# Kernel optimization log

Measured on AMD Instinct MI355X. Metric: run time of the kernel, lower is better.

Reference implementation:

```python
import jax, jax.numpy as jnp
import numpy as np

# Model dims (from init_kwargs + mamba_ssm defaults)
D_MODEL = 1024
N_LAYER = 2
D_STATE = 16
D_CONV = 4
D_INNER = 2 * D_MODEL          # expand=2
DT_RANK = D_MODEL // 16        # 64
VOCAB = 32000
BATCH, SEQLEN = 2, 1024


def setup_inputs() -> dict:
    key = jax.random.key(0)
    ks = jax.random.split(key, 10)
    s = 0.02
    x = jax.random.randint(ks[0], (BATCH, SEQLEN), 0, VOCAB)
    embedding = jax.random.normal(ks[1], (VOCAB, D_MODEL), dtype=jnp.float32) * s
    norm_w = jnp.ones((N_LAYER, D_MODEL), dtype=jnp.float32)
    in_proj_w = jax.random.normal(ks[2], (N_LAYER, 2 * D_INNER, D_MODEL), dtype=jnp.float32) * s
    conv_w = jax.random.normal(ks[3], (N_LAYER, D_INNER, D_CONV), dtype=jnp.float32) * (1.0 / np.sqrt(D_CONV))
    conv_b = jnp.zeros((N_LAYER, D_INNER), dtype=jnp.float32)
    x_proj_w = jax.random.normal(ks[4], (N_LAYER, DT_RANK + 2 * D_STATE, D_INNER), dtype=jnp.float32) * s
    dt_proj_w = jax.random.normal(ks[5], (N_LAYER, D_INNER, DT_RANK), dtype=jnp.float32) * (DT_RANK ** -0.5)
    # inverse-softplus of dt_init ~ 0.01 (mamba default dt range)
    dt_bias = jnp.full((N_LAYER, D_INNER), float(np.log(np.expm1(0.01))), dtype=jnp.float32)
    A_log = jnp.log(jnp.broadcast_to(jnp.arange(1, D_STATE + 1, dtype=jnp.float32), (N_LAYER, D_INNER, D_STATE)))
    D = jnp.ones((N_LAYER, D_INNER), dtype=jnp.float32)
    out_proj_w = jax.random.normal(ks[6], (N_LAYER, D_MODEL, D_INNER), dtype=jnp.float32) * s
    final_norm_w = jnp.ones((D_MODEL,), dtype=jnp.float32)
    return {"x": x, "embedding": embedding, "norm_w": norm_w, "in_proj_w": in_proj_w,
            "conv_w": conv_w, "conv_b": conv_b, "x_proj_w": x_proj_w, "dt_proj_w": dt_proj_w,
            "dt_bias": dt_bias, "A_log": A_log, "D": D, "out_proj_w": out_proj_w,
            "final_norm_w": final_norm_w}


def _rmsnorm(h, w, eps=1e-5):
    return h * jax.lax.rsqrt(jnp.mean(h * h, axis=-1, keepdims=True) + eps) * w


def _scan_combine(c1, c2):
    a1, b1 = c1
    a2, b2 = c2
    return a2 * a1, a2 * b1 + b2


def _mamba_block(h, norm_w, in_proj_w, conv_w, conv_b, x_proj_w, dt_proj_w, dt_bias, A_log, D, out_proj_w):
    u = _rmsnorm(h, norm_w)
    xz = jnp.einsum('bld,ed->ble', u, in_proj_w)           # [B,L,2*D_INNER]
    xi, z = jnp.split(xz, 2, axis=-1)
    # depthwise causal conv1d, kernel D_CONV
    k = conv_w.T[:, None, :]                               # [D_CONV, 1, D_INNER]
    xc = jax.lax.conv_general_dilated(xi, k, (1,), [(D_CONV - 1, 0)],
                                      dimension_numbers=('NLC', 'LIO', 'NLC'),
                                      feature_group_count=D_INNER) + conv_b
    xc = jax.nn.silu(xc)
    dbl = jnp.einsum('bld,ed->ble', xc, x_proj_w)          # [B,L,DT_RANK+2*D_STATE]
    dt_low = dbl[..., :DT_RANK]
    Bm = dbl[..., DT_RANK:DT_RANK + D_STATE]
    Cm = dbl[..., DT_RANK + D_STATE:]
    dt = jax.nn.softplus(jnp.einsum('blr,dr->bld', dt_low, dt_proj_w) + dt_bias)
    A = -jnp.exp(A_log)                                    # [D_INNER, D_STATE]
    a = jnp.exp(dt[..., None] * A)                         # [B,L,D_INNER,D_STATE]
    b = dt[..., None] * Bm[:, :, None, :] * xc[..., None]  # [B,L,D_INNER,D_STATE]
    hs = jax.lax.associative_scan(_scan_combine, (a, b), axis=1)[1]
    y = jnp.einsum('bldn,bln->bld', hs, Cm) + xc * D
    y = y * jax.nn.silu(z)
    return h + jnp.einsum('bld,md->blm', y, out_proj_w)


def reference(x, embedding, norm_w, in_proj_w, conv_w, conv_b, x_proj_w, dt_proj_w,
              dt_bias, A_log, D, out_proj_w, final_norm_w):
    h = embedding[x]                                       # [B,L,D_MODEL]
    for i in range(N_LAYER):
        h = _mamba_block(h, norm_w[i], in_proj_w[i], conv_w[i], conv_b[i], x_proj_w[i],
                         dt_proj_w[i], dt_bias[i], A_log[i], D[i], out_proj_w[i])
    h = _rmsnorm(h, final_norm_w)
    logits = jnp.einsum('bld,vd->blv', h, embedding)       # tied lm head
    return logits
```

## Files before the change

kernel.cpp:

```cpp
#include <hip/hip_runtime.h>
#include <hip/hip_bf16.h>
#include <math.h>

#define D_MODEL 1024
#define N_LAYER 2
#define D_STATE 16
#define D_CONV  4
#define D_INNER 2048
#define DT_RANK 64
#define VOCAB   32000
#define BATCH   2
#define SEQLEN  1024
#define TOKENS  (BATCH*SEQLEN)
#define NC      64
#define CL      16
#define XPZ     16

typedef __hip_bfloat16 bf16;
typedef __bf16 bf16x8 __attribute__((ext_vector_type(8)));
typedef float f32x4 __attribute__((ext_vector_type(4)));

__device__ inline void gld_lds16(const bf16* g, bf16* l) {
    __builtin_amdgcn_global_load_lds(
        (const __attribute__((address_space(1))) void*)g,
        (__attribute__((address_space(3))) void*)l, 16, 0, 0);
}

__device__ inline float softplus_fast(float v) {
    return (v > 20.f) ? v : __logf(1.f + __expf(v));
}
__device__ inline float silu_fast(float v) {
    return v / (1.f + __expf(-v));
}
__device__ inline float bfu(unsigned short s) {
    unsigned u = ((unsigned)s) << 16;
    float f;
    __builtin_memcpy(&f, &u, 4);
    return f;
}

__global__ __launch_bounds__(256) void embed_rms(const int* __restrict__ x,
                                                 const float* __restrict__ emb,
                                                 const float* __restrict__ w,
                                                 float* __restrict__ h,
                                                 bf16* __restrict__ u) {
    int t = blockIdx.x;
    int tok = x[t];
    float4 v = ((const float4*)(emb + (size_t)tok * D_MODEL))[threadIdx.x];
    ((float4*)(h + (size_t)t * D_MODEL))[threadIdx.x] = v;
    float ss = v.x*v.x + v.y*v.y + v.z*v.z + v.w*v.w;
    #pragma unroll
    for (int off = 32; off > 0; off >>= 1) ss += __shfl_down(ss, off);
    __shared__ float red[4];
    int lane = threadIdx.x & 63, wid = threadIdx.x >> 6;
    if (lane == 0) red[wid] = ss;
    __syncthreads();
    float tot = red[0] + red[1] + red[2] + red[3];
    float scale = rsqrtf(tot * (1.0f / (float)D_MODEL) + 1e-5f);
    float4 wq = ((const float4*)w)[threadIdx.x];
    size_t o = (size_t)t * D_MODEL + threadIdx.x * 4;
    u[o+0] = __float2bfloat16(v.x * scale * wq.x);
    u[o+1] = __float2bfloat16(v.y * scale * wq.y);
    u[o+2] = __float2bfloat16(v.z * scale * wq.z);
    u[o+3] = __float2bfloat16(v.w * scale * wq.w);
}

__global__ __launch_bounds__(256) void f32_to_bf16(const float* __restrict__ s,
                                                   bf16* __restrict__ d, int n) {
    int i = (blockIdx.x * 256 + threadIdx.x) * 4;
    if (i < n) {
        float4 v = *(const float4*)(s + i);
        d[i+0] = __float2bfloat16(v.x);
        d[i+1] = __float2bfloat16(v.y);
        d[i+2] = __float2bfloat16(v.z);
        d[i+3] = __float2bfloat16(v.w);
    }
}

__global__ __launch_bounds__(256) void conv_xproj_pad(const float* __restrict__ s,
                                                      bf16* __restrict__ d) {
    int col = blockIdx.x * 256 + threadIdx.x;
    int row = blockIdx.y;
    int layer = blockIdx.z;
    float v = (row < 96) ? s[((size_t)layer * 96 + row) * D_INNER + col] : 0.f;
    d[((size_t)layer * 128 + row) * D_INNER + col] = __float2bfloat16(v);
}

__global__ __launch_bounds__(256) void gemm_bf16(
    const bf16* __restrict__ A, int lda,
    const bf16* __restrict__ W, int ldw,
    float* __restrict__ C, int ldc,
    int N, int K, int acc, int swz, int M, int bfout)
{
    __shared__ bf16 lds[2][2][128 * 64];
    int bx = blockIdx.x, by = blockIdx.y;
    if (swz) {
        int bid = by * gridDim.x + bx;
        int q = (gridDim.x * gridDim.y) >> 3;
        int n = (bid & 7) * q + (bid >> 3);
        by = n % gridDim.y;
        bx = n / gridDim.y;
    }
    const int z = blockIdx.z;
    A += (size_t)z * K;
    W += (size_t)z * K;
    float* Cf = C + (size_t)z * M * (size_t)ldc;
    bf16*  Cb = (bf16*)C + (size_t)z * M * (size_t)ldc;

    const int tid  = threadIdx.x;
    const int wave = tid >> 6;
    const int lane = tid & 63;
    const int wr = wave >> 1, wc = wave & 1;
    const size_t rowBase = (size_t)by * 128;
    const size_t colBase = (size_t)bx * 128;

    const int srow = 8 * wave + (lane >> 3);
    const int scol = ((lane & 7) ^ (lane >> 3)) << 3;
    const bf16* aGs = A + (rowBase + srow) * (size_t)lda + scol;
    const bf16* bGs = W + (colBase + srow) * (size_t)ldw + scol;

#define STAGE(tt, bb) do {                                                      \
        const size_t kofs_ = (size_t)(tt) * 64;                                 \
        _Pragma("unroll")                                                       \
        for (int i_ = 0; i_ < 4; ++i_) {                                        \
            gld_lds16(aGs + kofs_ + (size_t)(32 * i_) * lda,                    \
                      &lds[bb][0][(32 * i_ + 8 * wave) * 64]);                  \
            gld_lds16(bGs + kofs_ + (size_t)(32 * i_) * ldw,                    \
                      &lds[bb][1][(32 * i_ + 8 * wave) * 64]);                  \
        }                                                                       \
    } while (0)

    f32x4 accv[4][4];
    #pragma unroll
    for (int i = 0; i < 4; ++i)
        #pragma unroll
        for (int j = 0; j < 4; ++j)
            accv[i][j] = f32x4{0.f, 0.f, 0.f, 0.f};

    const int arow0 = wr * 64 + (lane & 15);
    const int brow0 = wc * 64 + (lane & 15);
    const int h8  = (lane >> 4) << 3;
    const int sw8 = (lane & 7) << 3;

    const int NT = K >> 6;
    STAGE(0, 0);
    for (int t = 0; t < NT; ++t) {
        const int cur = t & 1;
        if (t + 1 < NT) {
            STAGE(t + 1, cur ^ 1);
            asm volatile("s_waitcnt vmcnt(8)" ::: "memory");
        } else {
            asm volatile("s_waitcnt vmcnt(0)" ::: "memory");
        }
        __builtin_amdgcn_s_barrier();

        const bf16* Ab = &lds[cur][0][0];
        const bf16* Bb = &lds[cur][1][0];
        #pragma unroll
        for (int kk = 0; kk < 2; ++kk) {
            const int cs = ((kk << 5) + h8) ^ sw8;
            bf16x8 af[4], bv[4];
            #pragma unroll
            for (int i = 0; i < 4; ++i)
                af[i] = *(const bf16x8*)(Ab + (arow0 + 16 * i) * 64 + cs);
            #pragma unroll
            for (int j = 0; j < 4; ++j)
                bv[j] = *(const bf16x8*)(Bb + (brow0 + 16 * j) * 64 + cs);
            #pragma unroll
            for (int i = 0; i < 4; ++i)
                #pragma unroll
                for (int j = 0; j < 4; ++j)
                    accv[i][j] = __builtin_amdgcn_mfma_f32_16x16x32_bf16(
                        af[i], bv[j], accv[i][j], 0, 0, 0);
        }
        asm volatile("s_waitcnt lgkmcnt(0)" ::: "memory");
        __builtin_amdgcn_s_barrier();
    }
#undef STAGE

    const int cl = lane & 15;
    const int rg = (lane >> 4) * 4;
    #pragma unroll
    for (int i = 0; i < 4; ++i) {
        #pragma unroll
        for (int j = 0; j < 4; ++j) {
            int col = (int)colBase + wc * 64 + j * 16 + cl;
            if (col < N) {
                size_t base = (rowBase + wr * 64 + i * 16 + rg) * (size_t)ldc + col;
                if (bfout) {
                    #pragma unroll
                    for (int r = 0; r < 4; ++r)
                        Cb[base + (size_t)r * ldc] = __float2bfloat16(accv[i][j][r]);
                } else {
                    #pragma unroll
                    for (int r = 0; r < 4; ++r) {
                        size_t idx = base + (size_t)r * ldc;
                        Cf[idx] = acc ? Cf[idx] + accv[i][j][r] : accv[i][j][r];
                    }
                }
            }
        }
    }
}

__global__ __launch_bounds__(512) void gemm_wide3(
    const bf16* __restrict__ A,
    const bf16* __restrict__ W,
    float* __restrict__ C, int ldc, int bfout)
{
    __shared__ bf16 ldsA[3][256 * 32];
    __shared__ bf16 ldsB[3][128 * 32];
    int bx = blockIdx.x, by = blockIdx.y;
    {
        int bid = by * gridDim.x + bx;
        int n = (bid & 7) * ((gridDim.x * gridDim.y) >> 3) + (bid >> 3);
        by = n & 7;
        bx = n >> 3;
    }
    const int tid  = threadIdx.x;
    const int wave = tid >> 6;
    const int lane = tid & 63;
    const int wr = wave >> 1;
    const int wc = wave & 1;
    const size_t rowBase = (size_t)by * 256;
    const size_t colBase = (size_t)bx * 128;

    const int srow   = lane >> 2;
    const int schunk = ((lane & 3) ^ ((lane >> 3) & 3)) << 3;
    const bf16* aG0 = A + (rowBase + 16 * wave       + srow) * (size_t)D_MODEL + schunk;
    const bf16* aG1 = A + (rowBase + 128 + 16 * wave + srow) * (size_t)D_MODEL + schunk;
    const bf16* bG  = W + (colBase + 16 * wave       + srow) * (size_t)D_MODEL + schunk;

#define STAGEW(tt, sAp, sBp) do {                                               \
        const size_t ko_ = (size_t)(tt) * 32;                                   \
        gld_lds16(aG0 + ko_, (sAp) + 512 * wave);                               \
        gld_lds16(aG1 + ko_, (sAp) + 512 * (8 + wave));                         \
        gld_lds16(bG  + ko_, (sBp) + 512 * wave);                               \
    } while (0)

    f32x4 accv[4][4];
    #pragma unroll
    for (int i = 0; i < 4; ++i)
        #pragma unroll
        for (int j = 0; j < 4; ++j)
            accv[i][j] = f32x4{0.f, 0.f, 0.f, 0.f};

    const int l15 = lane & 15;
    const int cs = (((lane >> 4) ^ ((l15 >> 1) & 3)) << 3);
    const int arow0 = wr * 64 + l15;
    const int brow0 = wc * 64 + l15;

    STAGEW(0, &ldsA[0][0], &ldsB[0][0]);
    STAGEW(1, &ldsA[1][0], &ldsB[1][0]);

    int rs = 0, ps = 2;
    #pragma unroll 1
    for (int t = 0; t < 32; ++t) {
        if (t < 31) { asm volatile("s_waitcnt vmcnt(3)" ::: "memory"); }
        else        { asm volatile("s_waitcnt vmcnt(0)" ::: "memory"); }
        __builtin_amdgcn_s_barrier();
        __builtin_amdgcn_sched_barrier(0);

        if (t + 2 < 32) STAGEW(t + 2, &ldsA[ps][0], &ldsB[ps][0]);

        const bf16* Ab = &ldsA[rs][0];
        const bf16* Bb = &ldsB[rs][0];
        bf16x8 af[4], bv[4];
        #pragma unroll
        for (int i = 0; i < 4; ++i)
            af[i] = *(const bf16x8*)(Ab + (arow0 + 16 * i) * 32 + cs);
        #pragma unroll
        for (int j = 0; j < 4; ++j)
            bv[j] = *(const bf16x8*)(Bb + (brow0 + 16 * j) * 32 + cs);
        #pragma unroll
        for (int i = 0; i < 4; ++i)
            #pragma unroll
            for (int j = 0; j < 4; ++j)
                accv[i][j] = __builtin_amdgcn_mfma_f32_16x16x32_bf16(
                    af[i], bv[j], accv[i][j], 0, 0, 0);

        rs = (rs == 2) ? 0 : rs + 1;
        ps = (ps == 2) ? 0 : ps + 1;
    }
#undef STAGEW

    const int cl = l15;
    const int rg = (lane >> 4) * 4;
    #pragma unroll
    for (int i = 0; i < 4; ++i) {
        #pragma unroll
        for (int j = 0; j < 4; ++j) {
            int col = (int)colBase + wc * 64 + j * 16 + cl;
            size_t base = (rowBase + wr * 64 + i * 16 + rg) * (size_t)ldc + col;
            if (bfout) {
                bf16* Cb = (bf16*)C;
                #pragma unroll
                for (int r = 0; r < 4; ++r)
                    Cb[base + (size_t)r * ldc] = __float2bfloat16(accv[i][j][r]);
            } else {
                #pragma unroll
                for (int r = 0; r < 4; ++r)
                    C[base + (size_t)r * ldc] = accv[i][j][r];
            }
        }
    }
}

__global__ __launch_bounds__(256) void conv_silu_kernel(const bf16* __restrict__ xz,
                                                        const float* __restrict__ cw,
                                                        const float* __restrict__ cb,
                                                        bf16* __restrict__ xcb) {
    int d = blockIdx.x * 256 + threadIdx.x;
    int l0 = blockIdx.y * 8;
    int b = blockIdx.z;
    float w0 = cw[d*4+0], w1 = cw[d*4+1], w2 = cw[d*4+2], w3 = cw[d*4+3];
    float bias = cb[d];
    float win0 = (l0 >= 3) ? __bfloat162float(xz[((size_t)b * SEQLEN + l0 - 3) * (2*D_INNER) + d]) : 0.f;
    float win1 = (l0 >= 2) ? __bfloat162float(xz[((size_t)b * SEQLEN + l0 - 2) * (2*D_INNER) + d]) : 0.f;
    float win2 = (l0 >= 1) ? __bfloat162float(xz[((size_t)b * SEQLEN + l0 - 1) * (2*D_INNER) + d]) : 0.f;
    #pragma unroll
    for (int i = 0; i < 8; ++i) {
        float cur = __bfloat162float(xz[((size_t)b * SEQLEN + l0 + i) * (2*D_INNER) + d]);
        float acc = bias + w0*win0 + w1*win1 + w2*win2 + w3*cur;
        float s = silu_fast(acc);
        xcb[((size_t)b * SEQLEN + l0 + i) * D_INNER + d] = __float2bfloat16(s);
        win0 = win1; win1 = win2; win2 = cur;
    }
}

__global__ __launch_bounds__(256) void reduce_xproj(const float* __restrict__ px,
                                                    bf16* __restrict__ dbl_b) {
    int i = blockIdx.x * 256 + threadIdx.x;
    float s = 0.f;
    #pragma unroll
    for (int z = 0; z < XPZ; ++z) s += px[(size_t)z * (TOKENS*96) + i];
    dbl_b[i] = __float2bfloat16(s);
}

__global__ __launch_bounds__(256) void reduce_oproj_rms(const bf16* __restrict__ po,
                                                        float* __restrict__ h,
                                                        const float* __restrict__ w,
                                                        bf16* __restrict__ u) {
    int t = blockIdx.x;
    size_t base = (size_t)t * D_MODEL + threadIdx.x * 4;
    ushort4 ua = *(const ushort4*)(po + base);
    ushort4 ub = *(const ushort4*)(po + (size_t)TOKENS * D_MODEL + base);
    float4 hv = *(const float4*)(h + base);
    hv.x += bfu(ua.x) + bfu(ub.x);
    hv.y += bfu(ua.y) + bfu(ub.y);
    hv.z += bfu(ua.z) + bfu(ub.z);
    hv.w += bfu(ua.w) + bfu(ub.w);
    *(float4*)(h + base) = hv;
    float ss = hv.x*hv.x + hv.y*hv.y + hv.z*hv.z + hv.w*hv.w;
    #pragma unroll
    for (int off = 32; off > 0; off >>= 1) ss += __shfl_down(ss, off);
    __shared__ float red[4];
    int lane = threadIdx.x & 63, wid = threadIdx.x >> 6;
    if (lane == 0) red[wid] = ss;
    __syncthreads();
    float tot = red[0] + red[1] + red[2] + red[3];
    float scale = rsqrtf(tot * (1.0f / (float)D_MODEL) + 1e-5f);
    float4 wq = ((const float4*)w)[threadIdx.x];
    u[base+0] = __float2bfloat16(hv.x * scale * wq.x);
    u[base+1] = __float2bfloat16(hv.y * scale * wq.y);
    u[base+2] = __float2bfloat16(hv.z * scale * wq.z);
    u[base+3] = __float2bfloat16(hv.w * scale * wq.w);
}

__global__ __launch_bounds__(256) void scan_chunk(const bf16* __restrict__ dtp,
                                                  const float* __restrict__ dt_bias,
                                                  const bf16* __restrict__ dbl,
                                                  const bf16* __restrict__ xc,
                                                  const float* __restrict__ A_log,
                                                  float* __restrict__ dts_out,
                                                  bf16* __restrict__ sfin) {
    int d = blockIdx.x * 256 + threadIdx.x;
    int c = blockIdx.y;
    int b = blockIdx.z;
    __shared__ float Bs[CL][D_STATE];
    {
        int i = threadIdx.x;
        int l = i >> 4, n = i & 15;
        Bs[l][n] = __bfloat162float(dbl[((size_t)b * SEQLEN + c * CL + l) * 96 + DT_RANK + n]);
    }
    __syncthreads();
    float A[D_STATE];
    #pragma unroll
    for (int n = 0; n < D_STATE; ++n) A[n] = -__expf(A_log[d * D_STATE + n]);
    float bias = dt_bias[d];
    float st[D_STATE];
    #pragma unroll
    for (int n = 0; n < D_STATE; ++n) st[n] = 0.f;
    float dts = 0.f;
    for (int l = 0; l < CL; ++l) {
        size_t t = (size_t)b * SEQLEN + c * CL + l;
        float dtv = softplus_fast(__bfloat162float(dtp[t * D_INNER + d]) + bias);
        dts += dtv;
        float dx = dtv * __bfloat162float(xc[t * D_INNER + d]);
        #pragma unroll
        for (int n = 0; n < D_STATE; ++n) {
            float a = __expf(dtv * A[n]);
            st[n] = a * st[n] + dx * Bs[l][n];
        }
    }
    dts_out[((size_t)b * NC + c) * D_INNER + d] = dts;
    #pragma unroll
    for (int n = 0; n < D_STATE; ++n) {
        size_t o = (((size_t)b * NC + c) * D_STATE + n) * D_INNER + d;
        sfin[o] = __float2bfloat16(st[n]);
    }
}

__global__ __launch_bounds__(256) void scan_carry(const float* __restrict__ dts,
                                                  const bf16* __restrict__ sfin,
                                                  const float* __restrict__ A_log,
                                                  bf16* __restrict__ initS) {
    int idx = blockIdx.x * 256 + threadIdx.x;
    int d = idx & (D_INNER - 1);
    int n = (idx >> 11) & (D_STATE - 1);
    int b = idx >> 15;
    float A = -__expf(A_log[d * D_STATE + n]);
    float st = 0.f;
    for (int c = 0; c < NC; ++c) {
        size_t o = (((size_t)b * NC + c) * D_STATE + n) * D_INNER + d;
        initS[o] = __float2bfloat16(st);
        float ap = __expf(dts[((size_t)b * NC + c) * D_INNER + d] * A);
        st = ap * st + __bfloat162float(sfin[o]);
    }
}

__global__ __launch_bounds__(256) void scan_emit(const bf16* __restrict__ dtp,
                                                 const float* __restrict__ dt_bias,
                                                 const bf16* __restrict__ dbl,
                                                 const bf16* __restrict__ xc,
                                                 const bf16* __restrict__ xz,
                                                 const float* __restrict__ A_log,
                                                 const float* __restrict__ Dp,
                                                 const bf16* __restrict__ initS,
                                                 bf16* __restrict__ y) {
    int d = blockIdx.x * 256 + threadIdx.x;
    int c = blockIdx.y;
    int b = blockIdx.z;
    __shared__ float BCs[CL][2 * D_STATE];
    for (int i = threadIdx.x; i < CL * 2 * D_STATE; i += 256) {
        int l = i >> 5, n = i & 31;
        BCs[l][n] = __bfloat162float(dbl[((size_t)b * SEQLEN + c * CL + l) * 96 + DT_RANK + n]);
    }
    __syncthreads();
    float A[D_STATE];
    #pragma unroll
    for (int n = 0; n < D_STATE; ++n) A[n] = -__expf(A_log[d * D_STATE + n]);
    float bias = dt_bias[d];
    float Dv = Dp[d];
    float st[D_STATE];
    #pragma unroll
    for (int n = 0; n < D_STATE; ++n)
        st[n] = __bfloat162float(initS[(((size_t)b * NC + c) * D_STATE + n) * D_INNER + d]);
    for (int l = 0; l < CL; ++l) {
        size_t t = (size_t)b * SEQLEN + c * CL + l;
        float dtv = softplus_fast(__bfloat162float(dtp[t * D_INNER + d]) + bias);
        float xcv = __bfloat162float(xc[t * D_INNER + d]);
        float dx = dtv * xcv;
        float acc = 0.f;
        #pragma unroll
        for (int n = 0; n < D_STATE; ++n) {
            float a = __expf(dtv * A[n]);
            st[n] = a * st[n] + dx * BCs[l][n];
            acc += st[n] * BCs[l][D_STATE + n];
        }
        acc += xcv * Dv;
        float zv = __bfloat162float(xz[t * (2 * D_INNER) + D_INNER + d]);
        y[t * D_INNER + d] = __float2bfloat16(acc * silu_fast(zv));
    }
}

extern "C" void kernel_launch(void* const* d_in, const int* in_sizes, int n_in,
                              void* d_out, int out_size, void* d_ws, size_t ws_size,
                              hipStream_t stream) {
    const int*   x          = (const int*)  d_in[0];
    const float* emb        = (const float*)d_in[1];
    const float* norm_w     = (const float*)d_in[2];
    const float* in_proj_w  = (const float*)d_in[3];
    const float* conv_w     = (const float*)d_in[4];
    const float* conv_b     = (const float*)d_in[5];
    const float* x_proj_w   = (const float*)d_in[6];
    const float* dt_proj_w  = (const float*)d_in[7];
    const float* dt_bias    = (const float*)d_in[8];
    const float* A_log      = (const float*)d_in[9];
    const float* Dp         = (const float*)d_in[10];
    const float* out_proj_w = (const float*)d_in[11];
    const float* fnorm_w    = (const float*)d_in[12];
    float* out = (float*)d_out;
    float* ws  = (float*)d_ws;

    bf16*  embf   = (bf16*)ws;
    bf16*  u_b    = (bf16*)(ws + 16384000);
    bf16*  xz_b   = (bf16*)(ws + 17432576);
    bf16*  dtp_b  = (bf16*)(ws + 25821184);
    bf16*  xc_b   = (bf16*)(ws + 30015488);
    float* h      = ws + 36306944;
    bf16*  dbl_b  = (bf16*)(ws + 38600704);
    bf16*  y_b    = (bf16*)(ws + 38699008);
    bf16*  inpj_b = (bf16*)(ws + 40796160);
    bf16*  xpj_b  = (bf16*)(ws + 44990464);
    bf16*  dtpj_b = (bf16*)(ws + 45252608);
    bf16*  otpj_b = (bf16*)(ws + 45383680);
    float* dts    = ws + 47480832;
    bf16*  sfin   = (bf16*)(ws + 49577984);
    bf16*  initS  = (bf16*)(ws + 51675136);
    float* px     = ws + 53772288;
    bf16*  po_b   = (bf16*)(ws + 56918016);

    f32_to_bf16<<<(VOCAB*D_MODEL/4 + 255)/256, 256, 0, stream>>>(emb, embf, VOCAB*D_MODEL);
    f32_to_bf16<<<(2*2*D_INNER*D_MODEL/4 + 255)/256, 256, 0, stream>>>(in_proj_w,  inpj_b, 2*2*D_INNER*D_MODEL);
    conv_xproj_pad<<<dim3(D_INNER/256, 128, N_LAYER), 256, 0, stream>>>(x_proj_w, xpj_b);
    f32_to_bf16<<<(2*D_INNER*DT_RANK/4 + 255)/256, 256, 0, stream>>>(dt_proj_w,  dtpj_b, 2*D_INNER*DT_RANK);
    f32_to_bf16<<<(2*D_MODEL*D_INNER/4 + 255)/256, 256, 0, stream>>>(out_proj_w, otpj_b, 2*D_MODEL*D_INNER);

    embed_rms<<<TOKENS, 256, 0, stream>>>(x, emb, norm_w, h, u_b);

    for (int layer = 0; layer < N_LAYER; ++layer) {
        gemm_wide3<<<dim3(4096/128, TOKENS/256), 512, 0, stream>>>(
            u_b, inpj_b + (size_t)layer * 2 * D_INNER * D_MODEL,
            (float*)xz_b, 2 * D_INNER, 1);
        conv_silu_kernel<<<dim3(D_INNER/256, SEQLEN/8, BATCH), 256, 0, stream>>>(
            xz_b, conv_w + (size_t)layer * D_INNER * D_CONV, conv_b + layer * D_INNER,
            xc_b);
        gemm_bf16<<<dim3(1, TOKENS/128, XPZ), 256, 0, stream>>>(
            xc_b, D_INNER, xpj_b + (size_t)layer * 128 * D_INNER, D_INNER,
            px, 96, 96, 128, 0, 0, TOKENS, 0);
        reduce_xproj<<<(TOKENS*96)/256, 256, 0, stream>>>(px, dbl_b);
        gemm_bf16<<<dim3(D_INNER/128, TOKENS/128), 256, 0, stream>>>(
            dbl_b, 96, dtpj_b + (size_t)layer * D_INNER * DT_RANK, DT_RANK,
            (float*)dtp_b, D_INNER, D_INNER, DT_RANK, 0, 1, TOKENS, 1);
        scan_chunk<<<dim3(D_INNER/256, NC, BATCH), 256, 0, stream>>>(
            dtp_b, dt_bias + layer * D_INNER, dbl_b, xc_b,
            A_log + (size_t)layer * D_INNER * D_STATE, dts, sfin);
        scan_carry<<<(BATCH*D_STATE*D_INNER)/256, 256, 0, stream>>>(
            dts, sfin, A_log + (size_t)layer * D_INNER * D_STATE, initS);
        scan_emit<<<dim3(D_INNER/256, NC, BATCH), 256, 0, stream>>>(
            dtp_b, dt_bias + layer * D_INNER, dbl_b, xc_b, xz_b,
            A_log + (size_t)layer * D_INNER * D_STATE, Dp + layer * D_INNER,
            initS, y_b);
        gemm_bf16<<<dim3(D_MODEL/128, TOKENS/128, 2), 256, 0, stream>>>(
            y_b, D_INNER, otpj_b + (size_t)layer * D_MODEL * D_INNER, D_INNER,
            (float*)po_b, D_MODEL, D_MODEL, 1024, 0, 1, TOKENS, 1);
        reduce_oproj_rms<<<TOKENS, 256, 0, stream>>>(
            po_b, h, (layer + 1 < N_LAYER) ? (norm_w + (layer + 1) * D_MODEL) : fnorm_w,
            u_b);
    }

    gemm_wide3<<<dim3(VOCAB/128, TOKENS/256), 512, 0, stream>>>(u_b, embf, out, VOCAB, 0);
}
```

Measured before the change: 512.6 us.

## Fuse fp32-to-bf16 weight conversion into the wide GEMM B-tile loads

Removes the separate f32_to_bf16 passes over the embedding table and in_proj weights. The wide GEMM now stages fp32 weight tiles straight into LDS and converts them to bf16 in registers before the MFMAs. This saves writing and re-reading the bf16 copies (about 131MB of embedding conversion traffic alone). In exchange, each GEMM reads twice the weight bytes per tile and uses more LDS per stage, so the pipeline drops from three stages to two, with an extra barrier per iteration.

```diff
diff --git a/kernel.cpp b/kernel.cpp
--- a/kernel.cpp
+++ b/kernel.cpp
@@ -25,6 +25,11 @@
         (const __attribute__((address_space(1))) void*)g,
         (__attribute__((address_space(3))) void*)l, 16, 0, 0);
 }
+__device__ inline void gld_lds16f(const float* g, float* l) {
+    __builtin_amdgcn_global_load_lds(
+        (const __attribute__((address_space(1))) void*)g,
+        (__attribute__((address_space(3))) void*)l, 16, 0, 0);
+}
 
 __device__ inline float softplus_fast(float v) {
     return (v > 20.f) ? v : __logf(1.f + __expf(v));
@@ -37,6 +42,12 @@
     float f;
     __builtin_memcpy(&f, &u, 4);
     return f;
+}
+__device__ inline bf16x8 cvt8v(f32x4 a, f32x4 b) {
+    bf16x8 r;
+    r[0] = (__bf16)a[0]; r[1] = (__bf16)a[1]; r[2] = (__bf16)a[2]; r[3] = (__bf16)a[3];
+    r[4] = (__bf16)b[0]; r[5] = (__bf16)b[1]; r[6] = (__bf16)b[2]; r[7] = (__bf16)b[3];
+    return r;
 }
 
 __global__ __launch_bounds__(256) void embed_rms(const int* __restrict__ x,
@@ -203,13 +214,13 @@
     }
 }
 
-__global__ __launch_bounds__(512) void gemm_wide3(
+__global__ __launch_bounds__(512) void gemm_wf32(
     const bf16* __restrict__ A,
-    const bf16* __restrict__ W,
+    const float* __restrict__ W,
     float* __restrict__ C, int ldc, int bfout)
 {
-    __shared__ bf16 ldsA[3][256 * 32];
-    __shared__ bf16 ldsB[3][128 * 32];
+    __shared__ bf16  ldsA[2][256 * 32];
+    __shared__ float ldsB[2][128 * 32];
     int bx = blockIdx.x, by = blockIdx.y;
     {
         int bid = by * gridDim.x + bx;
@@ -225,17 +236,21 @@
     const size_t rowBase = (size_t)by * 256;
     const size_t colBase = (size_t)bx * 128;
 
-    const int srow   = lane >> 2;
-    const int schunk = ((lane & 3) ^ ((lane >> 3) & 3)) << 3;
-    const bf16* aG0 = A + (rowBase + 16 * wave       + srow) * (size_t)D_MODEL + schunk;
-    const bf16* aG1 = A + (rowBase + 128 + 16 * wave + srow) * (size_t)D_MODEL + schunk;
-    const bf16* bG  = W + (colBase + 16 * wave       + srow) * (size_t)D_MODEL + schunk;
-
-#define STAGEW(tt, sAp, sBp) do {                                               \
+    const int srowA   = lane >> 2;
+    const int schunkA = ((lane & 3) ^ ((lane >> 3) & 3)) << 3;
+    const bf16* aG0 = A + (rowBase + 16 * wave       + srowA) * (size_t)D_MODEL + schunkA;
+    const bf16* aG1 = A + (rowBase + 128 + 16 * wave + srowA) * (size_t)D_MODEL + schunkA;
+    const int srowB   = lane >> 3;
+    const int schunkB = ((lane & 7) ^ (lane >> 3)) << 2;
+    const float* bG0 = W + (colBase + 16 * wave     + srowB) * (size_t)D_MODEL + schunkB;
+    const float* bG1 = W + (colBase + 16 * wave + 8 + srowB) * (size_t)D_MODEL + schunkB;
+
+#define STGF(tt, sl) do {                                                       \
         const size_t ko_ = (size_t)(tt) * 32;                                   \
-        gld_lds16(aG0 + ko_, (sAp) + 512 * wave);                               \
-        gld_lds16(aG1 + ko_, (sAp) + 512 * (8 + wave));                         \
-        gld_lds16(bG  + ko_, (sBp) + 512 * wave);                               \
+        gld_lds16(aG0 + ko_,  &ldsA[sl][512 * wave]);                           \
+        gld_lds16(aG1 + ko_,  &ldsA[sl][512 * (8 + wave)]);                     \
+        gld_lds16f(bG0 + ko_, &ldsB[sl][(16 * wave) * 32]);                     \
+        gld_lds16f(bG1 + ko_, &ldsB[sl][(16 * wave + 8) * 32]);                 \
     } while (0)
 
     f32x4 accv[4][4];
@@ -246,32 +261,38 @@
             accv[i][j] = f32x4{0.f, 0.f, 0.f, 0.f};
 
     const int l15 = lane & 15;
-    const int cs = (((lane >> 4) ^ ((l15 >> 1) & 3)) << 3);
+    const int hh  = lane >> 4;
+    const int csA = ((hh ^ ((l15 >> 1) & 3)) << 3);
+    const int rkB = l15 & 7;
+    const int c0B = (2 * hh) ^ rkB;
     const int arow0 = wr * 64 + l15;
     const int brow0 = wc * 64 + l15;
 
-    STAGEW(0, &ldsA[0][0], &ldsB[0][0]);
-    STAGEW(1, &ldsA[1][0], &ldsB[1][0]);
-
-    int rs = 0, ps = 2;
+    STGF(0, 0);
     #pragma unroll 1
     for (int t = 0; t < 32; ++t) {
-        if (t < 31) { asm volatile("s_waitcnt vmcnt(3)" ::: "memory"); }
-        else        { asm volatile("s_waitcnt vmcnt(0)" ::: "memory"); }
+        const int cur = t & 1;
+        if (t + 1 < 32) {
+            STGF(t + 1, cur ^ 1);
+            asm volatile("s_waitcnt vmcnt(4)" ::: "memory");
+        } else {
+            asm volatile("s_waitcnt vmcnt(0)" ::: "memory");
+        }
         __builtin_amdgcn_s_barrier();
-        __builtin_amdgcn_sched_barrier(0);
-
-        if (t + 2 < 32) STAGEW(t + 2, &ldsA[ps][0], &ldsB[ps][0]);
-
-        const bf16* Ab = &ldsA[rs][0];
-        const bf16* Bb = &ldsB[rs][0];
+
+        const bf16*  Ab = &ldsA[cur][0];
+        const float* Bb = &ldsB[cur][0];
         bf16x8 af[4], bv[4];
         #pragma unroll
         for (int i = 0; i < 4; ++i)
-            af[i] = *(const bf16x8*)(Ab + (arow0 + 16 * i) * 32 + cs);
-        #pragma unroll
-        for (int j = 0; j < 4; ++j)
-            bv[j] = *(const bf16x8*)(Bb + (brow0 + 16 * j) * 32 + cs);
+            af[i] = *(const bf16x8*)(Ab + (arow0 + 16 * i) * 32 + csA);
+        #pragma unroll
+        for (int j = 0; j < 4; ++j) {
+            int Rb = (brow0 + 16 * j) * 32;
+            f32x4 q0 = *(const f32x4*)(Bb + Rb + c0B * 4);
+            f32x4 q1 = *(const f32x4*)(Bb + Rb + (c0B ^ 1) * 4);
+            bv[j] = cvt8v(q0, q1);
+        }
         #pragma unroll
         for (int i = 0; i < 4; ++i)
             #pragma unroll
@@ -279,10 +300,10 @@
                 accv[i][j] = __builtin_amdgcn_mfma_f32_16x16x32_bf16(
                     af[i], bv[j], accv[i][j], 0, 0, 0);
 
-        rs = (rs == 2) ? 0 : rs + 1;
-        ps = (ps == 2) ? 0 : ps + 1;
-    }
-#undef STAGEW
+        asm volatile("s_waitcnt lgkmcnt(0)" ::: "memory");
+        __builtin_amdgcn_s_barrier();
+    }
+#undef STGF
 
     const int cl = l15;
     const int rg = (lane >> 4) * 4;
@@ -493,7 +514,6 @@
     float* out = (float*)d_out;
     float* ws  = (float*)d_ws;
 
-    bf16*  embf   = (bf16*)ws;
     bf16*  u_b    = (bf16*)(ws + 16384000);
     bf16*  xz_b   = (bf16*)(ws + 17432576);
     bf16*  dtp_b  = (bf16*)(ws + 25821184);
@@ -501,7 +521,6 @@
     float* h      = ws + 36306944;
     bf16*  dbl_b  = (bf16*)(ws + 38600704);
     bf16*  y_b    = (bf16*)(ws + 38699008);
-    bf16*  inpj_b = (bf16*)(ws + 40796160);
     bf16*  xpj_b  = (bf16*)(ws + 44990464);
     bf16*  dtpj_b = (bf16*)(ws + 45252608);
     bf16*  otpj_b = (bf16*)(ws + 45383680);
@@ -511,8 +530,6 @@
     float* px     = ws + 53772288;
     bf16*  po_b   = (bf16*)(ws + 56918016);
 
-    f32_to_bf16<<<(VOCAB*D_MODEL/4 + 255)/256, 256, 0, stream>>>(emb, embf, VOCAB*D_MODEL);
-    f32_to_bf16<<<(2*2*D_INNER*D_MODEL/4 + 255)/256, 256, 0, stream>>>(in_proj_w,  inpj_b, 2*2*D_INNER*D_MODEL);
     conv_xproj_pad<<<dim3(D_INNER/256, 128, N_LAYER), 256, 0, stream>>>(x_proj_w, xpj_b);
     f32_to_bf16<<<(2*D_INNER*DT_RANK/4 + 255)/256, 256, 0, stream>>>(dt_proj_w,  dtpj_b, 2*D_INNER*DT_RANK);
     f32_to_bf16<<<(2*D_MODEL*D_INNER/4 + 255)/256, 256, 0, stream>>>(out_proj_w, otpj_b, 2*D_MODEL*D_INNER);
@@ -520,8 +537,8 @@
     embed_rms<<<TOKENS, 256, 0, stream>>>(x, emb, norm_w, h, u_b);
 
     for (int layer = 0; layer < N_LAYER; ++layer) {
-        gemm_wide3<<<dim3(4096/128, TOKENS/256), 512, 0, stream>>>(
-            u_b, inpj_b + (size_t)layer * 2 * D_INNER * D_MODEL,
+        gemm_wf32<<<dim3(4096/128, TOKENS/256), 512, 0, stream>>>(
+            u_b, in_proj_w + (size_t)layer * 2 * D_INNER * D_MODEL,
             (float*)xz_b, 2 * D_INNER, 1);
         conv_silu_kernel<<<dim3(D_INNER/256, SEQLEN/8, BATCH), 256, 0, stream>>>(
             xz_b, conv_w + (size_t)layer * D_INNER * D_CONV, conv_b + layer * D_INNER,
@@ -550,5 +567,5 @@
             u_b);
     }
 
-    gemm_wide3<<<dim3(VOCAB/128, TOKENS/256), 512, 0, stream>>>(u_b, embf, out, VOCAB, 0);
-}
+    gemm_wf32<<<dim3(VOCAB/128, TOKENS/256), 512, 0, stream>>>(u_b, emb, out, VOCAB, 0);
+}
```

After: 554.0 us. 8.1% more time.
